# Performance work log

Hardware: AMD Instinct MI355X
Metric: run time of the kernel (lower is better)

Reference implementation:

```python
import jax, jax.numpy as jnp
import numpy as np

E = 8        # n_routed_experts
K = 4        # num_experts_per_tok
T = 1024     # tokens
H = 1024     # hidden_size
I = 1408     # moe_intermediate_size


def setup_inputs() -> dict:
    key = jax.random.key(0)
    ks = jax.random.split(key, 6)
    hidden_states = jax.random.normal(ks[0], (T, H), jnp.float32)
    rw = jax.random.uniform(ks[1], (T, K), jnp.float32)
    router_weights = rw / jnp.sum(rw, axis=-1, keepdims=True)  # normalized top-k router weights
    selected_experts = jax.random.randint(ks[2], (T, K), 0, E, jnp.int32)
    gate_w = jax.random.normal(ks[3], (E, H, I), jnp.float32) * (H ** -0.5)  # lecun_normal-ish
    up_w = jax.random.normal(ks[4], (E, H, I), jnp.float32) * (H ** -0.5)
    down_w = jax.random.normal(ks[5], (E, I, H), jnp.float32) * (I ** -0.5)
    return {
        'hidden_states': hidden_states,
        'router_weights': router_weights,
        'gate_w': gate_w,
        'up_w': up_w,
        'down_w': down_w,
        'selected_experts': selected_experts,
    }


def _grouped_matmul(x, w, seg):
    # x: [m, k] tokens sorted by expert; w: [E, k, n]; seg: [m] expert id per row.
    # Grouped GEMM expressed as E masked GEMMs (fixed small loop over experts);
    # a custom kernel would do true variable-group-size grouped GEMM.
    out = jnp.zeros((x.shape[0], w.shape[-1]), x.dtype)
    for e in range(w.shape[0]):
        out = out + jnp.where((seg == e)[:, None], x, jnp.zeros((), x.dtype)) @ w[e]
    return out


def reference(hidden_states, router_weights, gate_w, up_w, down_w, selected_experts):
    t, k = selected_experts.shape
    flat = selected_experts.ravel()                       # [t*k]
    hs = jnp.repeat(hidden_states, k, axis=0)             # [t*k, H]
    sort_idx = jnp.argsort(flat)                          # dispatch: sort tokens by expert
    seg = flat[sort_idx]
    xs = hs[sort_idx]
    gate = _grouped_matmul(xs, gate_w, seg)               # [t*k, I]
    up = _grouped_matmul(xs, up_w, seg)                   # [t*k, I]
    h = jax.nn.silu(gate) * up                            # fused SwiGLU
    down = _grouped_matmul(h, down_w, seg)                # [t*k, H]
    unsort = jnp.argsort(sort_idx)                        # scatter back to token order
    out = down[unsort].reshape(t, k, -1)
    return jnp.sum(out * router_weights[..., None], axis=1)  # weighted combine [t, H]
```

## Files before the change

### kernel.cpp

```cpp
#include <hip/hip_runtime.h>
#include <hip/hip_bf16.h>
#include <cstdint>
#include <cstddef>

#define NE 8
#define NT 1024
#define NK 4
#define NH 1024
#define NI 1408
#define NA (NT * NK)
#define BM 128
#define MAXTILES 40
#define PADSLOTS 5120

typedef short short8 __attribute__((ext_vector_type(8)));
typedef float f32x4 __attribute__((ext_vector_type(4)));
typedef float f4v __attribute__((ext_vector_type(4)));
typedef unsigned short u16;

#define WS_HDR   0
#define WS_SORT  1024
#define WS_XBF   21504
#define WS_GT    2118656
#define WS_UT    25187328
#define WS_DT    48256000
#define WS_HB    71324672
#define WS_DTMP  85742592

__device__ __forceinline__ u16 f2b(float f) {
  union { float f; uint32_t u; } c; c.f = f;
  uint32_t u = c.u;
  return (u16)((u + 0x7FFFu + ((u >> 16) & 1u)) >> 16);
}

__device__ __forceinline__ void llds16(const void* g, void* l) {
  __builtin_amdgcn_global_load_lds(
      (const __attribute__((address_space(1))) void*)g,
      (__attribute__((address_space(3))) void*)l, 16, 0, 0);
}

__global__ void bucket_kernel(const int* __restrict__ sel, int* __restrict__ hdr,
                              int* __restrict__ sorted) {
  __shared__ int cnt[NE], fill[NE], poff_s[NE + 1];
  int tid = threadIdx.x;
  if (tid < NE) { cnt[tid] = 0; fill[tid] = 0; }
  __syncthreads();
  for (int i = tid; i < NA; i += 256) atomicAdd(&cnt[sel[i]], 1);
  __syncthreads();
  if (tid == 0) {
    int off = 0, nt = 0;
    for (int e = 0; e < NE; ++e) {
      poff_s[e] = off;
      int tiles = (cnt[e] + BM - 1) / BM;
      for (int j = 0; j < tiles; ++j) { hdr[32 + nt] = e; hdr[80 + nt] = off + j * BM; ++nt; }
      off += tiles * BM;
    }
    poff_s[NE] = off;
    hdr[17] = nt;
    for (int e = 0; e < NE; ++e) hdr[e] = cnt[e];
    for (int e = 0; e <= NE; ++e) hdr[8 + e] = poff_s[e];
  }
  __syncthreads();
  for (int i = tid; i < PADSLOTS; i += 256) sorted[i] = -1;
  __syncthreads();
  for (int i = tid; i < NA; i += 256) {
    int e = sel[i];
    int p = atomicAdd(&fill[e], 1);
    sorted[poff_s[e] + p] = i;
  }
}

__global__ __launch_bounds__(256) void transcvt_all(
    const float* __restrict__ gw, const float* __restrict__ uw, const float* __restrict__ dw,
    const float* __restrict__ hs,
    u16* __restrict__ gT, u16* __restrict__ uT, u16* __restrict__ dT, u16* __restrict__ xbf) {
  int tid = threadIdx.x;
  int y = blockIdx.y;
  if (y == 24) {
    for (int i = blockIdx.x * 256 + tid; i * 4 < NT * NH; i += 176 * 256) {
      f4v v = __builtin_nontemporal_load((const f4v*)&hs[i * 4]);
      ushort4 o;
      o.x = f2b(v.x); o.y = f2b(v.y); o.z = f2b(v.z); o.w = f2b(v.w);
      *(ushort4*)&xbf[i * 4] = o;
    }
    return;
  }
  __shared__ u16 t2[2][64][72];
  int tensor = y >> 3, e = y & 7;
  const float* src; u16* dst; int K, N, kb, nb;
  if (tensor == 0)      { src = gw; dst = gT; }
  else if (tensor == 1) { src = uw; dst = uT; }
  else                  { src = dw; dst = dT; }
  if (tensor < 2) { K = NH; N = NI; nb = blockIdx.x % 11; kb = blockIdx.x / 11; }
  else            { K = NI; N = NH; nb = blockIdx.x % 8;  kb = blockIdx.x / 8;  }
  int k0 = kb * 64, n0 = nb * 128;
  src += (size_t)e * K * N;
  dst += (size_t)e * K * N;

  int r = tid >> 4, c = tid & 15;
  f4v v[2][4];
#pragma unroll
  for (int t = 0; t < 2; ++t)
#pragma unroll
    for (int i = 0; i < 4; ++i)
      v[t][i] = __builtin_nontemporal_load(
          (const f4v*)&src[(size_t)(k0 + r + 16 * i) * N + n0 + t * 64 + c * 4]);
#pragma unroll
  for (int t = 0; t < 2; ++t)
#pragma unroll
    for (int i = 0; i < 4; ++i) {
      ushort4 o;
      o.x = f2b(v[t][i].x); o.y = f2b(v[t][i].y); o.z = f2b(v[t][i].z); o.w = f2b(v[t][i].w);
      *(ushort4*)&t2[t][r + 16 * i][c * 4] = o;
    }
  __syncthreads();
#pragma unroll
  for (int t = 0; t < 2; ++t)
#pragma unroll
    for (int i = 0; i < 2; ++i) {
      int idx = i * 256 + tid;
      int n = idx >> 3, kc = idx & 7;
      u16 o[8];
#pragma unroll
      for (int j = 0; j < 8; ++j) o[j] = t2[t][kc * 8 + j][n];
      *(short8*)&dst[(size_t)(n0 + t * 64 + n) * K + k0 + kc * 8] = *(const short8*)o;
    }
}

__global__ __launch_bounds__(256, 4) void gemm1_kernel(
    const u16* __restrict__ xbf, const u16* __restrict__ gT, const u16* __restrict__ uT,
    u16* __restrict__ hbuf, const int* __restrict__ hdr, const int* __restrict__ sorted) {
  int tile = blockIdx.x;
  if (tile >= hdr[17]) return;
  int e = hdr[32 + tile];
  int slot0 = hdr[80 + tile];
  int n0 = blockIdx.y * 64;
  int tid = threadIdx.x;

  __shared__ u16 sA[128 * 64];
  __shared__ u16 sBg[64 * 64];
  __shared__ u16 sBu[64 * 64];

  const u16* aptr[4];
  for (int s = 0; s < 4; ++s) {
    int idx = s * 256 + tid;
    int row = idx >> 3, c = idx & 7;
    int kc = c ^ (row & 7);
    int as = sorted[slot0 + row];
    int trow = (as >= 0) ? (as >> 2) : 0;
    aptr[s] = xbf + (size_t)trow * NH + kc * 8;
  }
  const u16 *bgp[2], *bup[2];
  for (int s = 0; s < 2; ++s) {
    int idx = s * 256 + tid;
    int n = idx >> 3, c = idx & 7;
    int kc = c ^ (n & 7);
    size_t o = ((size_t)e * NI + n0 + n) * NH + kc * 8;
    bgp[s] = gT + o; bup[s] = uT + o;
  }

  int lane = tid & 63, wave = tid >> 6;
  int wm = wave >> 1, wn = wave & 1;
  int l15 = lane & 15, quad = lane >> 4;
  int sw = l15 & 7;

  f32x4 accg[4][2] = {}; f32x4 accu[4][2] = {};

  for (int kt = 0; kt < NH / 64; ++kt) {
    int ko = kt * 64;
    for (int s = 0; s < 4; ++s) llds16(aptr[s] + ko, &sA[(s * 256 + tid) * 8]);
    for (int s = 0; s < 2; ++s) {
      llds16(bgp[s] + ko, &sBg[(s * 256 + tid) * 8]);
      llds16(bup[s] + ko, &sBu[(s * 256 + tid) * 8]);
    }
    __syncthreads();
    for (int ks = 0; ks < 2; ++ks) {
      int pos = ((ks * 4 + quad) ^ sw) * 8;
      short8 av[4], bg[2], bu[2];
      for (int mf = 0; mf < 4; ++mf)
        av[mf] = *(const short8*)&sA[(wm * 64 + mf * 16 + l15) * 64 + pos];
      for (int nf = 0; nf < 2; ++nf) {
        bg[nf] = *(const short8*)&sBg[(wn * 32 + nf * 16 + l15) * 64 + pos];
        bu[nf] = *(const short8*)&sBu[(wn * 32 + nf * 16 + l15) * 64 + pos];
      }
      for (int mf = 0; mf < 4; ++mf)
        for (int nf = 0; nf < 2; ++nf) {
          accg[mf][nf] = __builtin_amdgcn_mfma_f32_16x16x32_bf16(av[mf], bg[nf], accg[mf][nf], 0, 0, 0);
          accu[mf][nf] = __builtin_amdgcn_mfma_f32_16x16x32_bf16(av[mf], bu[nf], accu[mf][nf], 0, 0, 0);
        }
    }
    __syncthreads();
  }

  for (int mf = 0; mf < 4; ++mf)
    for (int nf = 0; nf < 2; ++nf)
      for (int r = 0; r < 4; ++r) {
        int row = wm * 64 + mf * 16 + quad * 4 + r;
        int col = n0 + wn * 32 + nf * 16 + l15;
        float g = accg[mf][nf][r], u = accu[mf][nf][r];
        float hv = (g / (1.f + __expf(-g))) * u;
        hbuf[(size_t)(slot0 + row) * NI + col] = f2b(hv);
      }
}

__global__ __launch_bounds__(256, 4) void gemm2_kernel(
    const u16* __restrict__ hbuf, const u16* __restrict__ dT,
    float* __restrict__ dtmp, const int* __restrict__ hdr, const int* __restrict__ sorted) {
  int tile = blockIdx.x;
  if (tile >= hdr[17]) return;
  int e = hdr[32 + tile];
  int slot0 = hdr[80 + tile];
  int n0 = blockIdx.y * 128;
  int tid = threadIdx.x;

  __shared__ u16 sA[128 * 64];
  __shared__ u16 sB[128 * 64];

  const u16 *ap[4], *bp[4];
  for (int s = 0; s < 4; ++s) {
    int idx = s * 256 + tid;
    int r = idx >> 3, c = idx & 7;
    int kc = c ^ (r & 7);
    ap[s] = hbuf + (size_t)(slot0 + r) * NI + kc * 8;
    bp[s] = dT + ((size_t)e * NH + n0 + r) * NI + kc * 8;
  }

  int lane = tid & 63, wave = tid >> 6;
  int wm = wave >> 1, wn = wave & 1;
  int l15 = lane & 15, quad = lane >> 4;
  int sw = l15 & 7;

  f32x4 acc[4][4] = {};

  for (int kt = 0; kt < NI / 64; ++kt) {
    int ko = kt * 64;
    for (int s = 0; s < 4; ++s) llds16(ap[s] + ko, &sA[(s * 256 + tid) * 8]);
    for (int s = 0; s < 4; ++s) llds16(bp[s] + ko, &sB[(s * 256 + tid) * 8]);
    __syncthreads();
    for (int ks = 0; ks < 2; ++ks) {
      int pos = ((ks * 4 + quad) ^ sw) * 8;
      short8 av[4], bv[4];
      for (int mf = 0; mf < 4; ++mf)
        av[mf] = *(const short8*)&sA[(wm * 64 + mf * 16 + l15) * 64 + pos];
      for (int nf = 0; nf < 4; ++nf)
        bv[nf] = *(const short8*)&sB[(wn * 64 + nf * 16 + l15) * 64 + pos];
      for (int mf = 0; mf < 4; ++mf)
        for (int nf = 0; nf < 4; ++nf)
          acc[mf][nf] = __builtin_amdgcn_mfma_f32_16x16x32_bf16(av[mf], bv[nf], acc[mf][nf], 0, 0, 0);
    }
    __syncthreads();
  }

  for (int mf = 0; mf < 4; ++mf) {
    int rowb = wm * 64 + mf * 16 + quad * 4;
    for (int r = 0; r < 4; ++r) {
      int as = sorted[slot0 + rowb + r];
      if (as < 0) continue;
      float* orow = dtmp + (size_t)as * NH + n0 + wn * 64;
      for (int nf = 0; nf < 4; ++nf)
        orow[nf * 16 + l15] = acc[mf][nf][r];
    }
  }
}

__global__ void combine_kernel(const float* __restrict__ dtmp, const float* __restrict__ rw,
                               float* __restrict__ out) {
  int t = blockIdx.x;
  int c = threadIdx.x * 4;
  float4 acc = make_float4(0.f, 0.f, 0.f, 0.f);
  for (int k = 0; k < NK; ++k) {
    float w = rw[t * NK + k];
    float4 v = *(const float4*)&dtmp[(size_t)(t * NK + k) * NH + c];
    acc.x += w * v.x; acc.y += w * v.y; acc.z += w * v.z; acc.w += w * v.w;
  }
  *(float4*)&out[(size_t)t * NH + c] = acc;
}

extern "C" void kernel_launch(void* const* d_in, const int* in_sizes, int n_in,
                              void* d_out, int out_size, void* d_ws, size_t ws_size,
                              hipStream_t stream) {
  const float* hs  = (const float*)d_in[0];
  const float* rw  = (const float*)d_in[1];
  const float* gw  = (const float*)d_in[2];
  const float* uw  = (const float*)d_in[3];
  const float* dw  = (const float*)d_in[4];
  const int*   sel = (const int*)d_in[5];
  float* out = (float*)d_out;

  char* ws = (char*)d_ws;
  int*  hdr    = (int*)(ws + WS_HDR);
  int*  sorted = (int*)(ws + WS_SORT);
  u16*  xbf    = (u16*)(ws + WS_XBF);
  u16*  gT     = (u16*)(ws + WS_GT);
  u16*  uT     = (u16*)(ws + WS_UT);
  u16*  dT     = (u16*)(ws + WS_DT);
  u16*  hb     = (u16*)(ws + WS_HB);
  float* dtmp  = (float*)(ws + WS_DTMP);

  hipLaunchKernelGGL(bucket_kernel, dim3(1), dim3(256), 0, stream, sel, hdr, sorted);
  hipLaunchKernelGGL(transcvt_all, dim3(176, 25), dim3(256), 0, stream,
                     gw, uw, dw, hs, gT, uT, dT, xbf);
  hipLaunchKernelGGL(gemm1_kernel, dim3(MAXTILES, NI / 64), dim3(256), 0, stream, xbf, gT, uT, hb, hdr, sorted);
  hipLaunchKernelGGL(gemm2_kernel, dim3(MAXTILES, NH / 128), dim3(256), 0, stream, hb, dT, dtmp, hdr, sorted);
  hipLaunchKernelGGL(combine_kernel, dim3(NT), dim3(256), 0, stream, dtmp, rw, out);
}
```

Baseline: 248.5 us.

## Merge prep stages, overlap down-weight conversion with gemm1, atomic combine

Folds the bucket sort into the gate/up weight conversion kernel and moves the down-weight conversion and output zeroing into the gemm1 launch as extra blocks, so that work runs alongside gemm1. gemm2 now scales by router weights and atomically adds into the output, which removes the separate combine kernel and the fp32 intermediate buffer. This cuts the launch count from five to three and avoids a round trip through memory. In exchange, float atomics make summation order nondeterministic and add contention on output rows.

```diff
diff --git a/kernel.cpp b/kernel.cpp
--- a/kernel.cpp
+++ b/kernel.cpp
@@ -25,7 +25,6 @@
 #define WS_UT    25187328
 #define WS_DT    48256000
 #define WS_HB    71324672
-#define WS_DTMP  85742592
 
 __device__ __forceinline__ u16 f2b(float f) {
   union { float f; uint32_t u; } c; c.f = f;
@@ -39,44 +38,49 @@
       (__attribute__((address_space(3))) void*)l, 16, 0, 0);
 }
 
-__global__ void bucket_kernel(const int* __restrict__ sel, int* __restrict__ hdr,
-                              int* __restrict__ sorted) {
-  __shared__ int cnt[NE], fill[NE], poff_s[NE + 1];
-  int tid = threadIdx.x;
-  if (tid < NE) { cnt[tid] = 0; fill[tid] = 0; }
+__device__ __forceinline__ void transcvt_stripe(const float* __restrict__ src,
+                                                u16* __restrict__ dst,
+                                                int K, int N, int k0, int n0,
+                                                u16* smem, int tid) {
+  u16 (*t2)[64][72] = (u16(*)[64][72])smem;
+  int r = tid >> 4, c = tid & 15;
+  f4v v[2][4];
+#pragma unroll
+  for (int t = 0; t < 2; ++t)
+#pragma unroll
+    for (int i = 0; i < 4; ++i)
+      v[t][i] = __builtin_nontemporal_load(
+          (const f4v*)&src[(size_t)(k0 + r + 16 * i) * N + n0 + t * 64 + c * 4]);
+#pragma unroll
+  for (int t = 0; t < 2; ++t)
+#pragma unroll
+    for (int i = 0; i < 4; ++i) {
+      ushort4 o;
+      o.x = f2b(v[t][i].x); o.y = f2b(v[t][i].y); o.z = f2b(v[t][i].z); o.w = f2b(v[t][i].w);
+      *(ushort4*)&t2[t][r + 16 * i][c * 4] = o;
+    }
   __syncthreads();
-  for (int i = tid; i < NA; i += 256) atomicAdd(&cnt[sel[i]], 1);
-  __syncthreads();
-  if (tid == 0) {
-    int off = 0, nt = 0;
-    for (int e = 0; e < NE; ++e) {
-      poff_s[e] = off;
-      int tiles = (cnt[e] + BM - 1) / BM;
-      for (int j = 0; j < tiles; ++j) { hdr[32 + nt] = e; hdr[80 + nt] = off + j * BM; ++nt; }
-      off += tiles * BM;
-    }
-    poff_s[NE] = off;
-    hdr[17] = nt;
-    for (int e = 0; e < NE; ++e) hdr[e] = cnt[e];
-    for (int e = 0; e <= NE; ++e) hdr[8 + e] = poff_s[e];
-  }
-  __syncthreads();
-  for (int i = tid; i < PADSLOTS; i += 256) sorted[i] = -1;
-  __syncthreads();
-  for (int i = tid; i < NA; i += 256) {
-    int e = sel[i];
-    int p = atomicAdd(&fill[e], 1);
-    sorted[poff_s[e] + p] = i;
-  }
-}
-
-__global__ __launch_bounds__(256) void transcvt_all(
-    const float* __restrict__ gw, const float* __restrict__ uw, const float* __restrict__ dw,
-    const float* __restrict__ hs,
-    u16* __restrict__ gT, u16* __restrict__ uT, u16* __restrict__ dT, u16* __restrict__ xbf) {
+#pragma unroll
+  for (int t = 0; t < 2; ++t)
+#pragma unroll
+    for (int i = 0; i < 2; ++i) {
+      int idx = i * 256 + tid;
+      int n = idx >> 3, kc = idx & 7;
+      u16 o[8];
+#pragma unroll
+      for (int j = 0; j < 8; ++j) o[j] = t2[t][kc * 8 + j][n];
+      *(short8*)&dst[(size_t)(n0 + t * 64 + n) * K + k0 + kc * 8] = *(const short8*)o;
+    }
+}
+
+__global__ __launch_bounds__(256) void k1_prep(
+    const float* __restrict__ gw, const float* __restrict__ uw, const float* __restrict__ hs,
+    const int* __restrict__ sel,
+    u16* __restrict__ gT, u16* __restrict__ uT, u16* __restrict__ xbf,
+    int* __restrict__ hdr, int* __restrict__ sorted) {
   int tid = threadIdx.x;
   int y = blockIdx.y;
-  if (y == 24) {
+  if (y == 16) {
     for (int i = blockIdx.x * 256 + tid; i * 4 < NT * NH; i += 176 * 256) {
       f4v v = __builtin_nontemporal_load((const f4v*)&hs[i * 4]);
       ushort4 o;
@@ -85,61 +89,81 @@
     }
     return;
   }
-  __shared__ u16 t2[2][64][72];
+  if (y == 17) {
+    if (blockIdx.x != 0) return;
+    __shared__ int cnt[NE], fill[NE], poff_s[NE + 1];
+    if (tid < NE) { cnt[tid] = 0; fill[tid] = 0; }
+    __syncthreads();
+    for (int i = tid; i < NA; i += 256) atomicAdd(&cnt[sel[i]], 1);
+    __syncthreads();
+    if (tid == 0) {
+      int off = 0, nt = 0;
+      for (int e = 0; e < NE; ++e) {
+        poff_s[e] = off;
+        int tiles = (cnt[e] + BM - 1) / BM;
+        for (int j = 0; j < tiles; ++j) { hdr[32 + nt] = e; hdr[80 + nt] = off + j * BM; ++nt; }
+        off += tiles * BM;
+      }
+      poff_s[NE] = off;
+      hdr[17] = nt;
+      for (int e = 0; e < NE; ++e) hdr[e] = cnt[e];
+      for (int e = 0; e <= NE; ++e) hdr[8 + e] = poff_s[e];
+    }
+    __syncthreads();
+    for (int i = tid; i < PADSLOTS; i += 256) sorted[i] = -1;
+    __syncthreads();
+    for (int i = tid; i < NA; i += 256) {
+      int e = sel[i];
+      int p = atomicAdd(&fill[e], 1);
+      sorted[poff_s[e] + p] = i;
+    }
+    return;
+  }
+  __shared__ u16 smem[2 * 64 * 72];
   int tensor = y >> 3, e = y & 7;
-  const float* src; u16* dst; int K, N, kb, nb;
-  if (tensor == 0)      { src = gw; dst = gT; }
-  else if (tensor == 1) { src = uw; dst = uT; }
-  else                  { src = dw; dst = dT; }
-  if (tensor < 2) { K = NH; N = NI; nb = blockIdx.x % 11; kb = blockIdx.x / 11; }
-  else            { K = NI; N = NH; nb = blockIdx.x % 8;  kb = blockIdx.x / 8;  }
-  int k0 = kb * 64, n0 = nb * 128;
-  src += (size_t)e * K * N;
-  dst += (size_t)e * K * N;
-
-  int r = tid >> 4, c = tid & 15;
-  f4v v[2][4];
-#pragma unroll
-  for (int t = 0; t < 2; ++t)
-#pragma unroll
-    for (int i = 0; i < 4; ++i)
-      v[t][i] = __builtin_nontemporal_load(
-          (const f4v*)&src[(size_t)(k0 + r + 16 * i) * N + n0 + t * 64 + c * 4]);
-#pragma unroll
-  for (int t = 0; t < 2; ++t)
-#pragma unroll
-    for (int i = 0; i < 4; ++i) {
-      ushort4 o;
-      o.x = f2b(v[t][i].x); o.y = f2b(v[t][i].y); o.z = f2b(v[t][i].z); o.w = f2b(v[t][i].w);
-      *(ushort4*)&t2[t][r + 16 * i][c * 4] = o;
-    }
-  __syncthreads();
-#pragma unroll
-  for (int t = 0; t < 2; ++t)
-#pragma unroll
-    for (int i = 0; i < 2; ++i) {
-      int idx = i * 256 + tid;
-      int n = idx >> 3, kc = idx & 7;
-      u16 o[8];
-#pragma unroll
-      for (int j = 0; j < 8; ++j) o[j] = t2[t][kc * 8 + j][n];
-      *(short8*)&dst[(size_t)(n0 + t * 64 + n) * K + k0 + kc * 8] = *(const short8*)o;
-    }
-}
-
-__global__ __launch_bounds__(256, 4) void gemm1_kernel(
+  const float* src = (tensor == 0) ? gw : uw;
+  u16* dst = (tensor == 0) ? gT : uT;
+  src += (size_t)e * NH * NI;
+  dst += (size_t)e * NH * NI;
+  int nb = blockIdx.x % 11, kb = blockIdx.x / 11;
+  transcvt_stripe(src, dst, NH, NI, kb * 64, nb * 128, smem, tid);
+}
+
+__global__ __launch_bounds__(256, 4) void k2_gemm1(
     const u16* __restrict__ xbf, const u16* __restrict__ gT, const u16* __restrict__ uT,
-    u16* __restrict__ hbuf, const int* __restrict__ hdr, const int* __restrict__ sorted) {
-  int tile = blockIdx.x;
+    u16* __restrict__ hbuf, const int* __restrict__ hdr, const int* __restrict__ sorted,
+    const float* __restrict__ dw, u16* __restrict__ dT, float* __restrict__ outz) {
+  __shared__ u16 smem[16384];
+  int b = blockIdx.x;
+  int tid = threadIdx.x;
+
+  if (b >= 2288) {
+    int base = (b - 2288) * 16384;
+    f4v z = {0.f, 0.f, 0.f, 0.f};
+#pragma unroll
+    for (int i = 0; i < 16; ++i)
+      *(f4v*)&outz[base + (i * 256 + tid) * 4] = z;
+    return;
+  }
+  if (b >= 880) {
+    int idx = b - 880;
+    int e = idx / 176, stripe = idx % 176;
+    int nb = stripe % 8, kb = stripe / 8;
+    const float* src = dw + (size_t)e * NI * NH;
+    u16* dst = dT + (size_t)e * NI * NH;
+    transcvt_stripe(src, dst, NI, NH, kb * 64, nb * 128, smem, tid);
+    return;
+  }
+
+  int tile = b % 40;
   if (tile >= hdr[17]) return;
   int e = hdr[32 + tile];
   int slot0 = hdr[80 + tile];
-  int n0 = blockIdx.y * 64;
-  int tid = threadIdx.x;
-
-  __shared__ u16 sA[128 * 64];
-  __shared__ u16 sBg[64 * 64];
-  __shared__ u16 sBu[64 * 64];
+  int n0 = (b / 40) * 64;
+
+  u16* sA  = smem;
+  u16* sBg = smem + 8192;
+  u16* sBu = smem + 12288;
 
   const u16* aptr[4];
   for (int s = 0; s < 4; ++s) {
@@ -203,9 +227,10 @@
       }
 }
 
-__global__ __launch_bounds__(256, 4) void gemm2_kernel(
+__global__ __launch_bounds__(256, 4) void k3_gemm2(
     const u16* __restrict__ hbuf, const u16* __restrict__ dT,
-    float* __restrict__ dtmp, const int* __restrict__ hdr, const int* __restrict__ sorted) {
+    const float* __restrict__ rw, float* __restrict__ out,
+    const int* __restrict__ hdr, const int* __restrict__ sorted) {
   int tile = blockIdx.x;
   if (tile >= hdr[17]) return;
   int e = hdr[32 + tile];
@@ -256,24 +281,12 @@
     for (int r = 0; r < 4; ++r) {
       int as = sorted[slot0 + rowb + r];
       if (as < 0) continue;
-      float* orow = dtmp + (size_t)as * NH + n0 + wn * 64;
+      float w = rw[as];
+      float* orow = out + (size_t)(as >> 2) * NH + n0 + wn * 64;
       for (int nf = 0; nf < 4; ++nf)
-        orow[nf * 16 + l15] = acc[mf][nf][r];
-    }
-  }
-}
-
-__global__ void combine_kernel(const float* __restrict__ dtmp, const float* __restrict__ rw,
-                               float* __restrict__ out) {
-  int t = blockIdx.x;
-  int c = threadIdx.x * 4;
-  float4 acc = make_float4(0.f, 0.f, 0.f, 0.f);
-  for (int k = 0; k < NK; ++k) {
-    float w = rw[t * NK + k];
-    float4 v = *(const float4*)&dtmp[(size_t)(t * NK + k) * NH + c];
-    acc.x += w * v.x; acc.y += w * v.y; acc.z += w * v.z; acc.w += w * v.w;
-  }
-  *(float4*)&out[(size_t)t * NH + c] = acc;
+        atomicAdd(&orow[nf * 16 + l15], w * acc[mf][nf][r]);
+    }
+  }
 }
 
 extern "C" void kernel_launch(void* const* d_in, const int* in_sizes, int n_in,
@@ -295,12 +308,11 @@
   u16*  uT     = (u16*)(ws + WS_UT);
   u16*  dT     = (u16*)(ws + WS_DT);
   u16*  hb     = (u16*)(ws + WS_HB);
-  float* dtmp  = (float*)(ws + WS_DTMP);
-
-  hipLaunchKernelGGL(bucket_kernel, dim3(1), dim3(256), 0, stream, sel, hdr, sorted);
-  hipLaunchKernelGGL(transcvt_all, dim3(176, 25), dim3(256), 0, stream,
-                     gw, uw, dw, hs, gT, uT, dT, xbf);
-  hipLaunchKernelGGL(gemm1_kernel, dim3(MAXTILES, NI / 64), dim3(256), 0, stream, xbf, gT, uT, hb, hdr, sorted);
-  hipLaunchKernelGGL(gemm2_kernel, dim3(MAXTILES, NH / 128), dim3(256), 0, stream, hb, dT, dtmp, hdr, sorted);
-  hipLaunchKernelGGL(combine_kernel, dim3(NT), dim3(256), 0, stream, dtmp, rw, out);
-}
+
+  hipLaunchKernelGGL(k1_prep, dim3(176, 18), dim3(256), 0, stream,
+                     gw, uw, hs, sel, gT, uT, xbf, hdr, sorted);
+  hipLaunchKernelGGL(k2_gemm1, dim3(2352), dim3(256), 0, stream,
+                     xbf, gT, uT, hb, hdr, sorted, dw, dT, out);
+  hipLaunchKernelGGL(k3_gemm2, dim3(MAXTILES, NH / 128), dim3(256), 0, stream,
+                     hb, dT, rw, out, hdr, sorted);
+}
```

Result: no change. 247.8 us (-0.3%).
